# Optimization experiments

Measured on AMD Instinct MI355X. Metric: run time of the kernel, lower is better.

Reference implementation:

```python
import jax, jax.numpy as jnp
import numpy as np

N = 100000       # nodes
E = 3200000      # edges
F_IN = 512       # input features
H = 256          # hidden channels
C = 64           # classes
L = 8            # GCN2 layers
ALPHA = 0.1
THETA = 0.5


def setup_inputs() -> dict:
    key = jax.random.key(0)
    ks = jax.random.split(key, 8)
    x = jax.random.normal(ks[0], (N, F_IN), dtype=jnp.float32)
    edge_val = jax.random.uniform(ks[1], (E,), dtype=jnp.float32)
    W_in = jax.random.normal(ks[2], (F_IN, H), dtype=jnp.float32) * 0.05
    b_in = jnp.zeros((H,), dtype=jnp.float32)
    conv_W = jax.random.normal(ks[3], (L, H, H), dtype=jnp.float32) * 0.05
    W_out = jax.random.normal(ks[4], (H, C), dtype=jnp.float32) * 0.05
    b_out = jnp.zeros((C,), dtype=jnp.float32)
    edge_row = jax.random.randint(ks[5], (E,), 0, N, dtype=jnp.int32)
    edge_col = jax.random.randint(ks[6], (E,), 0, N, dtype=jnp.int32)
    return {"x": x, "edge_val": edge_val, "W_in": W_in, "b_in": b_in,
            "conv_W": conv_W, "W_out": W_out, "b_out": b_out,
            "edge_row": edge_row, "edge_col": edge_col}


def spmm(edge_row, edge_col, edge_val, feat):
    # out[r] = sum_{edges (r,c)} val * feat[c]  -- sparse adj @ dense feat
    msgs = feat[edge_col] * edge_val[:, None]          # [E, H]
    return jax.ops.segment_sum(msgs, edge_row, num_segments=N)


def reference(x, edge_val, W_in, b_in, conv_W, W_out, b_out, edge_row, edge_col):
    # input linear + relu (dropout p=0.0 -> identity)
    h = jax.nn.relu(x @ W_in + b_in)                   # [N, H]
    x0 = h
    for l in range(L):
        beta = np.log(THETA / (l + 1) + 1.0)
        agg = spmm(edge_row, edge_col, edge_val, h)    # A @ h
        mix = (1.0 - ALPHA) * agg + ALPHA * x0          # initial residual
        h = (1.0 - beta) * mix + beta * (mix @ conv_W[l])  # identity mapping
        h = jax.nn.relu(h)
    logits = h @ W_out + b_out                         # [N, C]
    return jax.nn.log_softmax(logits, axis=-1)
```

## Files before the change

kernel.cpp:

```cpp
#include <hip/hip_runtime.h>
#include <hip/hip_bf16.h>
#include <math.h>

#define NN 100000
#define EE 3200000
#define FIN 512
#define HH 256
#define CC 64
#define LL 8
#define SLOTS 80

#define BM 128
#define BN 128
#define BK 32
#define APAD 40

typedef __attribute__((ext_vector_type(8))) short bf16x8;
typedef __attribute__((ext_vector_type(4))) float f32x4;
typedef __attribute__((ext_vector_type(8))) unsigned short u16x8;

__device__ __forceinline__ float bf2f(ushort u) {
  union { unsigned int i; float f; } v; v.i = ((unsigned int)u) << 16; return v.f;
}
__device__ __forceinline__ ushort f2bf(float f) {
  union { float f; unsigned int i; } v; v.f = f;
  unsigned int x = v.i;
  return (ushort)((x + 0x7FFFu + ((x >> 16) & 1u)) >> 16);
}
__device__ __forceinline__ float i2f(int i) {
  union { int i; float f; } v; v.i = i; return v.f;
}

__global__ void k_detect(const ushort* __restrict__ xr, int* __restrict__ flag) {
  __shared__ int cs[256];
  int t = threadIdx.x; int c = 0;
  for (int j = 0; j < 16; j++) {
    ushort u = xr[(size_t)(t * 16 + j) * 2];
    int e = (u >> 7) & 0xFF;
    c += (e >= 90 && e <= 140) ? 1 : 0;
  }
  cs[t] = c; __syncthreads();
  for (int off = 128; off > 0; off >>= 1) {
    if (t < off) cs[t] += cs[t + off];
    __syncthreads();
  }
  if (t == 0) flag[0] = (cs[0] < 2458) ? 1 : 0;
}

__global__ void k_transpose(const void* __restrict__ src, const int* __restrict__ flag,
                            ushort* __restrict__ dst, int R, int C) {
  int f32 = flag[0];
  size_t base = (size_t)blockIdx.y * R * C;
  int idx = blockIdx.x * 256 + threadIdx.x;
  if (idx < R * C) {
    int r = idx / C, c = idx % C;
    ushort v;
    if (f32) v = f2bf(((const float*)src)[base + idx]);
    else     v = ((const ushort*)src)[base + idx];
    dst[base + (size_t)c * R + r] = v;
  }
}

#define SCB 1563
__global__ void k_scatter_ell(const int* __restrict__ row, const int* __restrict__ col,
                              const void* __restrict__ val, const int* __restrict__ flag,
                              int* __restrict__ cursor, int2* __restrict__ cpack) {
  int f32 = flag[0];
  int t = blockIdx.x * 256 + threadIdx.x;
  const int T = SCB * 256;
#pragma unroll
  for (int j = 0; j < 8; j++) {
    int e = t + j * T;
    if (e < EE) {
      int r = row[e];
      int p = atomicAdd(&cursor[r], 1);
      if (p < SLOTS) {
        int v = f32 ? ((const int*)val)[e]
                    : (int)(((unsigned)((const ushort*)val)[e]) << 16);
        cpack[(size_t)r * SLOTS + p] = make_int2(col[e], v);
      }
    }
  }
}

__global__ void k_spmm_mix(const int* __restrict__ deg, const int2* __restrict__ cpack,
                           const ushort* __restrict__ hsrc, const ushort* __restrict__ x0,
                           ushort* __restrict__ mix) {
  int wave = threadIdx.x >> 6, lane = threadIdx.x & 63;
  int r = blockIdx.x * 4 + wave;
  if (r >= NN) return;
  int cnt = deg[r]; if (cnt > SLOTS) cnt = SLOTS;
  const int2* base = cpack + (size_t)r * SLOTS;
  int half = lane >> 5;
  int f = (lane & 31) * 8;
  float acc[8];
#pragma unroll
  for (int j = 0; j < 8; j++) acc[j] = 0.f;

  int i = half;
  for (; i + 14 < cnt; i += 16) {
    int2 p[8]; u16x8 h[8];
#pragma unroll
    for (int q = 0; q < 8; q++) p[q] = base[i + 2 * q];
#pragma unroll
    for (int q = 0; q < 8; q++) h[q] = *(const u16x8*)(hsrc + (size_t)p[q].x * HH + f);
#pragma unroll
    for (int q = 0; q < 8; q++) {
      float v = i2f(p[q].y);
#pragma unroll
      for (int j = 0; j < 8; j++) acc[j] += v * bf2f(h[q][j]);
    }
  }
  for (; i < cnt; i += 2) {
    int2 p0 = base[i];
    u16x8 h0 = *(const u16x8*)(hsrc + (size_t)p0.x * HH + f);
    float v0 = i2f(p0.y);
#pragma unroll
    for (int j = 0; j < 8; j++) acc[j] += v0 * bf2f(h0[j]);
  }
#pragma unroll
  for (int j = 0; j < 8; j++) acc[j] += __shfl_xor(acc[j], 32, 64);

  if (half == 0) {
    u16x8 xv = *(const u16x8*)(x0 + (size_t)r * HH + f);
    u16x8 mv;
#pragma unroll
    for (int j = 0; j < 8; j++) mv[j] = f2bf(0.9f * acc[j] + 0.1f * bf2f(xv[j]));
    *(u16x8*)(mix + (size_t)r * HH + f) = mv;
  }
}

__global__ __launch_bounds__(256) void k_gemm_fast(
    const ushort* __restrict__ A, const ushort* __restrict__ Bt,
    const ushort* __restrict__ resid, float c0, float c1,
    ushort* __restrict__ outp, int M) {
  __shared__ ushort As[128 * 64];
  __shared__ ushort Bs[128 * 64];
  int tid = threadIdx.x;
  int i0 = blockIdx.y * 128, j0 = blockIdx.x * 128;
  int lane = tid & 63, wave = tid >> 6;
  int wm = (wave >> 1) * 64, wn = (wave & 1) * 64;
  int l15 = lane & 15, lq = lane >> 4;
  int srow = lane >> 3;
  int scol = (lane & 7) * 8;

  f32x4 acc[4][4];
  for (int a = 0; a < 4; a++) for (int b = 0; b < 4; b++)
    for (int c = 0; c < 4; c++) acc[a][b][c] = 0.f;

  for (int t = 0; t < 4; t++) {
    int k0 = t * 64;
    if (t) __syncthreads();
    for (int j = 0; j < 4; j++) {
      int chunk = wave * 4 + j;
      int arow = chunk * 8 + srow;
      const ushort* gA = A + (size_t)(i0 + arow) * 256 + k0 + scol;
      __builtin_amdgcn_global_load_lds(
          (const __attribute__((address_space(1))) void*)gA,
          (__attribute__((address_space(3))) void*)(As + chunk * 512), 16, 0, 0);
      const ushort* gB = Bt + (size_t)(j0 + arow) * 256 + k0 + scol;
      __builtin_amdgcn_global_load_lds(
          (const __attribute__((address_space(1))) void*)gB,
          (__attribute__((address_space(3))) void*)(Bs + chunk * 512), 16, 0, 0);
    }
    __syncthreads();
    for (int kh = 0; kh < 2; kh++) {
      bf16x8 af[4], bfr[4];
      for (int fm = 0; fm < 4; fm++)
        af[fm] = *(const bf16x8*)(As + (wm + fm * 16 + l15) * 64 + kh * 32 + lq * 8);
      for (int fn = 0; fn < 4; fn++)
        bfr[fn] = *(const bf16x8*)(Bs + (wn + fn * 16 + l15) * 64 + kh * 32 + lq * 8);
      for (int fm = 0; fm < 4; fm++)
        for (int fn = 0; fn < 4; fn++)
          acc[fm][fn] = __builtin_amdgcn_mfma_f32_16x16x32_bf16(af[fm], bfr[fn], acc[fm][fn], 0, 0, 0);
    }
  }
  for (int fm = 0; fm < 4; fm++) {
    int rbase = i0 + wm + fm * 16 + lq * 4;
    for (int fn = 0; fn < 4; fn++) {
      int gcol = j0 + wn + fn * 16 + l15;
      for (int rg = 0; rg < 4; rg++) {
        int row = rbase + rg;
        if (row < M) {
          float v = c1 * acc[fm][fn][rg];
          if (resid) v += c0 * bf2f(resid[(size_t)row * HH + gcol]);
          v = fmaxf(v, 0.f);
          outp[(size_t)row * HH + gcol] = f2bf(v);
        }
      }
    }
  }
}

__global__ __launch_bounds__(256) void k_gemm(
    const void* __restrict__ Aptr, int a_mode, const int* __restrict__ dflag, int lda,
    const ushort* __restrict__ Bt, int K,
    const ushort* __restrict__ resid, float c0, float c1,
    ushort* __restrict__ outp, int M) {
  __shared__ ushort Alds[BM * APAD];
  __shared__ ushort Blds[BN * APAD];
  int af32 = (a_mode == 2) ? dflag[0] : a_mode;
  int tid = threadIdx.x;
  int i0 = blockIdx.y * BM, j0 = blockIdx.x * BN;
  int lane = tid & 63, wave = tid >> 6;
  int wm = (wave >> 1) * 64, wn = (wave & 1) * 64;
  int l15 = lane & 15, lq = lane >> 4;

  f32x4 acc[4][4];
  for (int a = 0; a < 4; a++) for (int b = 0; b < 4; b++)
    for (int c = 0; c < 4; c++) acc[a][b][c] = 0.f;

  for (int k0 = 0; k0 < K; k0 += BK) {
    for (int u = tid; u < BM * 4; u += 256) {
      int m = u >> 2, kc = (u & 3) * 8;
      int row = i0 + m;
      u16x8 av;
      if (row < M) {
        if (af32) {
          const float* ap = (const float*)Aptr + (size_t)row * lda + k0 + kc;
          float4 f0 = *(const float4*)ap;
          float4 f1 = *(const float4*)(ap + 4);
          av[0] = f2bf(f0.x); av[1] = f2bf(f0.y); av[2] = f2bf(f0.z); av[3] = f2bf(f0.w);
          av[4] = f2bf(f1.x); av[5] = f2bf(f1.y); av[6] = f2bf(f1.z); av[7] = f2bf(f1.w);
        } else {
          av = *(const u16x8*)((const ushort*)Aptr + (size_t)row * lda + k0 + kc);
        }
      } else {
#pragma unroll
        for (int j = 0; j < 8; j++) av[j] = 0;
      }
      *(u16x8*)(Alds + m * APAD + kc) = av;
    }
    for (int u = tid; u < BN * 4; u += 256) {
      int n = u >> 2, kc = (u & 3) * 8;
      u16x8 bv = *(const u16x8*)(Bt + (size_t)(j0 + n) * K + k0 + kc);
      *(u16x8*)(Blds + n * APAD + kc) = bv;
    }
    __syncthreads();
    bf16x8 afrag[4], bfrag[4];
    for (int fm = 0; fm < 4; fm++)
      afrag[fm] = *(const bf16x8*)(Alds + (wm + fm * 16 + l15) * APAD + lq * 8);
    for (int fn = 0; fn < 4; fn++)
      bfrag[fn] = *(const bf16x8*)(Blds + (wn + fn * 16 + l15) * APAD + lq * 8);
    for (int fm = 0; fm < 4; fm++)
      for (int fn = 0; fn < 4; fn++)
        acc[fm][fn] = __builtin_amdgcn_mfma_f32_16x16x32_bf16(afrag[fm], bfrag[fn], acc[fm][fn], 0, 0, 0);
    __syncthreads();
  }
  for (int fm = 0; fm < 4; fm++) {
    int rbase = i0 + wm + fm * 16 + lq * 4;
    for (int fn = 0; fn < 4; fn++) {
      int gcol = j0 + wn + fn * 16 + l15;
      for (int rg = 0; rg < 4; rg++) {
        int row = rbase + rg;
        if (row < M) {
          float v = c1 * acc[fm][fn][rg];
          if (resid) v += c0 * bf2f(resid[(size_t)row * HH + gcol]);
          v = fmaxf(v, 0.f);
          outp[(size_t)row * HH + gcol] = f2bf(v);
        }
      }
    }
  }
}

__global__ __launch_bounds__(256) void k_head(
    const ushort* __restrict__ h, const ushort* __restrict__ Bt,
    const int* __restrict__ flag, void* __restrict__ outp, int M) {
  __shared__ float slog[BM * 65];
  ushort* Alds = (ushort*)slog;
  ushort* Blds = (ushort*)slog + BM * APAD;
  int f32o = flag[0];
  int tid = threadIdx.x;
  int i0 = blockIdx.x * BM;
  int lane = tid & 63, wave = tid >> 6;
  int l15 = lane & 15, lq = lane >> 4;

  f32x4 acc[2][4];
  for (int a = 0; a < 2; a++) for (int b = 0; b < 4; b++)
    for (int c = 0; c < 4; c++) acc[a][b][c] = 0.f;

  for (int k0 = 0; k0 < HH; k0 += BK) {
    for (int u = tid; u < BM * 4; u += 256) {
      int m = u >> 2, kc = (u & 3) * 8;
      int row = i0 + m;
      u16x8 av;
      if (row < M) av = *(const u16x8*)(h + (size_t)row * HH + k0 + kc);
      else {
#pragma unroll
        for (int j = 0; j < 8; j++) av[j] = 0;
      }
      *(u16x8*)(Alds + m * APAD + kc) = av;
    }
    for (int u = tid; u < CC * 4; u += 256) {
      int n = u >> 2, kc = (u & 3) * 8;
      u16x8 bv = *(const u16x8*)(Bt + (size_t)n * HH + k0 + kc);
      *(u16x8*)(Blds + n * APAD + kc) = bv;
    }
    __syncthreads();
    bf16x8 afrag[2], bfrag[4];
    for (int fm = 0; fm < 2; fm++)
      afrag[fm] = *(const bf16x8*)(Alds + (wave * 32 + fm * 16 + l15) * APAD + lq * 8);
    for (int fn = 0; fn < 4; fn++)
      bfrag[fn] = *(const bf16x8*)(Blds + (fn * 16 + l15) * APAD + lq * 8);
    for (int fm = 0; fm < 2; fm++)
      for (int fn = 0; fn < 4; fn++)
        acc[fm][fn] = __builtin_amdgcn_mfma_f32_16x16x32_bf16(afrag[fm], bfrag[fn], acc[fm][fn], 0, 0, 0);
    __syncthreads();
  }
  for (int fm = 0; fm < 2; fm++) {
    int rl = wave * 32 + fm * 16 + lq * 4;
    for (int fn = 0; fn < 4; fn++) {
      int col = fn * 16 + l15;
      for (int rg = 0; rg < 4; rg++)
        slog[(rl + rg) * 65 + col] = acc[fm][fn][rg];
    }
  }
  __syncthreads();
  if (tid < BM) {
    int grow = i0 + tid;
    if (grow < M) {
      float mx = -1e30f;
      for (int c = 0; c < CC; c++) mx = fmaxf(mx, slog[tid * 65 + c]);
      float sum = 0.f;
      for (int c = 0; c < CC; c++) sum += expf(slog[tid * 65 + c] - mx);
      float lse = mx + logf(sum);
      for (int c = 0; c < CC; c++) {
        float v = slog[tid * 65 + c] - lse;
        if (f32o) ((float*)outp)[(size_t)grow * CC + c] = v;
        else      ((ushort*)outp)[(size_t)grow * CC + c] = f2bf(v);
      }
    }
  }
}

extern "C" void kernel_launch(void* const* d_in, const int* in_sizes, int n_in,
                              void* d_out, int out_size, void* d_ws, size_t ws_size,
                              hipStream_t stream) {
  const void* x        = d_in[0];
  const void* edge_val = d_in[1];
  const void* W_in     = d_in[2];
  const void* conv_W   = d_in[4];
  const void* W_out    = d_in[5];
  const int*  edge_row = (const int*)d_in[7];
  const int*  edge_col = (const int*)d_in[8];

  char* ws = (char*)d_ws;
  size_t off = 0;
  auto alloc = [&](size_t bytes) { void* p = ws + off; off += (bytes + 255) & ~(size_t)255; return p; };

  ushort* mix     = (ushort*)alloc((size_t)NN * HH * 2);
  ushort* x0      = (ushort*)alloc((size_t)NN * HH * 2);
  ushort* hbuf    = (ushort*)alloc((size_t)NN * HH * 2);
  int2*   cpack   = (int2*)  alloc((size_t)NN * SLOTS * 8);
  int*    cursor  = (int*)   alloc((size_t)NN * 4);
  int*    flags   = (int*)   alloc(256);
  ushort* Wt_in   = (ushort*)alloc((size_t)FIN * HH * 2);
  ushort* Wt_conv = (ushort*)alloc((size_t)LL * HH * HH * 2);
  ushort* Wt_out  = (ushort*)alloc((size_t)HH * CC * 2);
  (void)in_sizes; (void)n_in; (void)out_size; (void)ws_size;

  k_detect<<<1, 256, 0, stream>>>((const ushort*)x, flags);

  k_transpose<<<dim3((FIN * HH + 255) / 256, 1), 256, 0, stream>>>(W_in, flags, Wt_in, FIN, HH);
  k_transpose<<<dim3((HH * HH + 255) / 256, LL), 256, 0, stream>>>(conv_W, flags, Wt_conv, HH, HH);
  k_transpose<<<dim3((HH * CC + 255) / 256, 1), 256, 0, stream>>>(W_out, flags, Wt_out, HH, CC);

  hipMemsetAsync(cursor, 0, (size_t)NN * 4, stream);
  k_scatter_ell<<<SCB, 256, 0, stream>>>(edge_row, edge_col, edge_val, flags, cursor, cpack);

  int gy = (NN + BM - 1) / BM;
  k_gemm<<<dim3(HH / BN, gy), 256, 0, stream>>>(x, 2, flags, FIN, Wt_in, FIN,
                                                nullptr, 0.f, 1.f, x0, NN);

  const ushort* src = x0;
  for (int l = 0; l < LL; l++) {
    k_spmm_mix<<<(NN + 3) / 4, 256, 0, stream>>>(cursor, cpack, src, x0, mix);
    float beta = logf(0.5f / (float)(l + 1) + 1.0f);
    k_gemm_fast<<<dim3(HH / BN, gy), 256, 0, stream>>>(mix, Wt_conv + (size_t)l * HH * HH,
                                                       mix, 1.0f - beta, beta, hbuf, NN);
    src = hbuf;
  }

  k_head<<<gy, 256, 0, stream>>>(hbuf, Wt_out, flags, d_out, NN);
}
```

Measured before the change: 2.941 ms.

## Split SpMM feature dimension into slices with four lanes per row

The SpMM kernel now splits the 256 hidden features into 8 slices of 32, one per blockIdx.x. Each row is handled by 4 lanes (8 bf16 each), so a wave covers 16 rows instead of one row split into two halves. Edge metadata is read with nontemporal 64-bit loads and the cross-half shuffle reduction is removed. The intent is more independent rows in flight, better latency hiding and smaller per-slice gather working sets. The cost is that each row's edge list is re-read 8 times, and each gather is only 64 bytes per row within a slice.

```diff
diff --git a/kernel.cpp b/kernel.cpp
--- a/kernel.cpp
+++ b/kernel.cpp
@@ -83,51 +83,55 @@
   }
 }
 
-__global__ void k_spmm_mix(const int* __restrict__ deg, const int2* __restrict__ cpack,
-                           const ushort* __restrict__ hsrc, const ushort* __restrict__ x0,
-                           ushort* __restrict__ mix) {
+__global__ __launch_bounds__(256) void k_spmm_mix(
+    const int* __restrict__ deg, const int2* __restrict__ cpack,
+    const ushort* __restrict__ hsrc, const ushort* __restrict__ x0,
+    ushort* __restrict__ mix) {
+  int slice = blockIdx.x;
   int wave = threadIdx.x >> 6, lane = threadIdx.x & 63;
-  int r = blockIdx.x * 4 + wave;
+  int r = blockIdx.y * 64 + wave * 16 + (lane >> 2);
   if (r >= NN) return;
+  int quad = lane & 3;
+  int fo = slice * 32 + quad * 8;
   int cnt = deg[r]; if (cnt > SLOTS) cnt = SLOTS;
-  const int2* base = cpack + (size_t)r * SLOTS;
-  int half = lane >> 5;
-  int f = (lane & 31) * 8;
+  const long long* base = (const long long*)(cpack + (size_t)r * SLOTS);
+
   float acc[8];
 #pragma unroll
   for (int j = 0; j < 8; j++) acc[j] = 0.f;
 
-  int i = half;
-  for (; i + 14 < cnt; i += 16) {
-    int2 p[8]; u16x8 h[8];
-#pragma unroll
-    for (int q = 0; q < 8; q++) p[q] = base[i + 2 * q];
-#pragma unroll
-    for (int q = 0; q < 8; q++) h[q] = *(const u16x8*)(hsrc + (size_t)p[q].x * HH + f);
+  int i = 0;
+  for (; i + 7 < cnt; i += 8) {
+    long long pq[8];
+#pragma unroll
+    for (int q = 0; q < 8; q++) pq[q] = __builtin_nontemporal_load(base + i + q);
+    u16x8 hv[8];
 #pragma unroll
     for (int q = 0; q < 8; q++) {
-      float v = i2f(p[q].y);
-#pragma unroll
-      for (int j = 0; j < 8; j++) acc[j] += v * bf2f(h[q][j]);
-    }
-  }
-  for (; i < cnt; i += 2) {
-    int2 p0 = base[i];
-    u16x8 h0 = *(const u16x8*)(hsrc + (size_t)p0.x * HH + f);
-    float v0 = i2f(p0.y);
-#pragma unroll
-    for (int j = 0; j < 8; j++) acc[j] += v0 * bf2f(h0[j]);
-  }
-#pragma unroll
-  for (int j = 0; j < 8; j++) acc[j] += __shfl_xor(acc[j], 32, 64);
-
-  if (half == 0) {
-    u16x8 xv = *(const u16x8*)(x0 + (size_t)r * HH + f);
-    u16x8 mv;
-#pragma unroll
-    for (int j = 0; j < 8; j++) mv[j] = f2bf(0.9f * acc[j] + 0.1f * bf2f(xv[j]));
-    *(u16x8*)(mix + (size_t)r * HH + f) = mv;
-  }
+      int c = (int)(unsigned)pq[q];
+      hv[q] = *(const u16x8*)(hsrc + (size_t)c * HH + fo);
+    }
+#pragma unroll
+    for (int q = 0; q < 8; q++) {
+      float v = i2f((int)(pq[q] >> 32));
+#pragma unroll
+      for (int j = 0; j < 8; j++) acc[j] += v * bf2f(hv[q][j]);
+    }
+  }
+  for (; i < cnt; i++) {
+    long long pq = __builtin_nontemporal_load(base + i);
+    int c = (int)(unsigned)pq;
+    u16x8 h0 = *(const u16x8*)(hsrc + (size_t)c * HH + fo);
+    float v = i2f((int)(pq >> 32));
+#pragma unroll
+    for (int j = 0; j < 8; j++) acc[j] += v * bf2f(h0[j]);
+  }
+
+  u16x8 xv = *(const u16x8*)(x0 + (size_t)r * HH + fo);
+  u16x8 mv;
+#pragma unroll
+  for (int j = 0; j < 8; j++) mv[j] = f2bf(0.9f * acc[j] + 0.1f * bf2f(xv[j]));
+  *(u16x8*)(mix + (size_t)r * HH + fo) = mv;
 }
 
 __global__ __launch_bounds__(256) void k_gemm_fast(
@@ -375,7 +379,7 @@
 
   const ushort* src = x0;
   for (int l = 0; l < LL; l++) {
-    k_spmm_mix<<<(NN + 3) / 4, 256, 0, stream>>>(cursor, cpack, src, x0, mix);
+    k_spmm_mix<<<dim3(8, (NN + 63) / 64), 256, 0, stream>>>(cursor, cpack, src, x0, mix);
     float beta = logf(0.5f / (float)(l + 1) + 1.0f);
     k_gemm_fast<<<dim3(HH / BN, gy), 256, 0, stream>>>(mix, Wt_conv + (size_t)l * HH * HH,
                                                        mix, 1.0f - beta, beta, hbuf, NN);
```

After: 4.809 ms. +63.5%, slower.
